# Kernel optimization log

Hardware: AMD Instinct MI355X
Metric: run time of the kernel (lower is better)

## Reference

```python
import jax, jax.numpy as jnp
import numpy as np

HID = 512
NUM_NODES = 100000
N_BATCH = 20000


def _gru_cell(x, h, W_ih, W_hh, b_ih, b_hh):
    # torch nn.GRU single-step cell; gate order r, z, n
    gi = x @ W_ih.T + b_ih            # [N, 3H]
    gh = h @ W_hh.T + b_hh            # [N, 3H]
    i_r, i_z, i_n = jnp.split(gi, 3, axis=-1)
    h_r, h_z, h_n = jnp.split(gh, 3, axis=-1)
    r = jax.nn.sigmoid(i_r + h_r)
    z = jax.nn.sigmoid(i_z + h_z)
    n = jnp.tanh(i_n + r * h_n)
    return (1.0 - z) * n + z * h


def setup_inputs() -> dict:
    key = jax.random.key(0)
    ks = jax.random.split(key, 12)
    s = 1.0 / np.sqrt(HID)
    inp = {
        'conv_emb': jax.random.normal(ks[0], (N_BATCH, HID), jnp.float32),
        'static_table': jax.random.normal(ks[1], (NUM_NODES, HID), jnp.float32),
        'dynamic_table': jax.random.normal(ks[2], (NUM_NODES, 2, HID), jnp.float32),
        'W_ih0': jax.random.normal(ks[3], (3 * HID, 2 * HID), jnp.float32) * s,
        'W_hh0': jax.random.normal(ks[4], (3 * HID, HID), jnp.float32) * s,
        'b_ih0': jax.random.normal(ks[5], (3 * HID,), jnp.float32) * s,
        'b_hh0': jax.random.normal(ks[6], (3 * HID,), jnp.float32) * s,
        'W_ih1': jax.random.normal(ks[7], (3 * HID, HID), jnp.float32) * s,
        'W_hh1': jax.random.normal(ks[8], (3 * HID, HID), jnp.float32) * s,
        'b_ih1': jax.random.normal(ks[9], (3 * HID,), jnp.float32) * s,
        'b_hh1': jax.random.normal(ks[10], (3 * HID,), jnp.float32) * s,
        'nids': jnp.arange(N_BATCH, dtype=jnp.int32),  # unique global node ids
    }
    return inp


def reference(conv_emb, static_table, dynamic_table,
              W_ih0, W_hh0, b_ih0, b_hh0,
              W_ih1, W_hh1, b_ih1, b_hh1, nids):
    # gather: static embeddings for batch nodes, concat with conv output
    x = jnp.concatenate([conv_emb, static_table[nids]], axis=-1)  # [N, 2H]
    h0 = dynamic_table[nids]                                      # [N, L, H]
    # single-step 2-layer GRU (seq_len == 1)
    h_new0 = _gru_cell(x, h0[:, 0], W_ih0, W_hh0, b_ih0, b_hh0)   # [N, H]
    h_new1 = _gru_cell(h_new0, h0[:, 1], W_ih1, W_hh1, b_ih1, b_hh1)
    hn = jnp.stack([h_new0, h_new1], axis=1)                      # [N, L, H]
    # scatter updated hidden states back into the persistent table
    updated_table = dynamic_table.at[nids].set(hn)                # [num_nodes, L, H]
    return updated_table
```

## Files before the change

### kernel.cpp

```cpp
#include <hip/hip_runtime.h>

#define NB 20000
#define NNODES 100000
#define MB2 79
#define MP2 (MB2*256)
#define NBITW 3125
#define NGEMM (MB2*8)
#define NCOPY 1416

typedef unsigned short u16;
typedef __bf16 bf16x8 __attribute__((ext_vector_type(8)));
typedef float f32x4 __attribute__((ext_vector_type(4)));

__device__ __forceinline__ u16 f2bf(float f) {
  union { float f; unsigned u; } v; v.f = f;
  unsigned r = v.u + 0x7fffu + ((v.u >> 16) & 1u);
  return (u16)(r >> 16);
}
__device__ __forceinline__ float bf2f(u16 b) {
  union { unsigned u; float f; } v; v.u = ((unsigned)b) << 16;
  return v.f;
}

template <int N> __device__ __forceinline__ void vmwaitc() {
  if constexpr (N == 0) asm volatile("s_waitcnt vmcnt(0)" ::: "memory");
  else if constexpr (N == 2) asm volatile("s_waitcnt vmcnt(2)" ::: "memory");
  else if constexpr (N == 4) asm volatile("s_waitcnt vmcnt(4)" ::: "memory");
  else asm volatile("s_waitcnt vmcnt(8)" ::: "memory");
  __builtin_amdgcn_sched_barrier(0);
}
__device__ __forceinline__ void bar() {
  __builtin_amdgcn_sched_barrier(0);
  __builtin_amdgcn_s_barrier();
  __builtin_amdgcn_sched_barrier(0);
}

__global__ void prep_bt0i(const float* __restrict__ Wih, const float* __restrict__ Whh,
                          u16* __restrict__ Bt) {
  int idx = blockIdx.x * 256 + threadIdx.x;
  if (idx >= 2048 * 384) return;
  int jg = idx / 384;
  int k = (idx % 384) * 4;
  int j = jg >> 2, g = jg & 3;
  float4 v = make_float4(0.f, 0.f, 0.f, 0.f);
  if (g < 2) {
    int row = g * 512 + j;
    v = (k < 1024) ? *(const float4*)(Wih + (size_t)row * 1024 + k)
                   : *(const float4*)(Whh + (size_t)row * 512 + (k - 1024));
  } else if (g == 2) {
    if (k < 1024) v = *(const float4*)(Wih + (size_t)(1024 + j) * 1024 + k);
  } else {
    if (k >= 1024) v = *(const float4*)(Whh + (size_t)(1024 + j) * 512 + (k - 1024));
  }
  ushort4 b; b.x = f2bf(v.x); b.y = f2bf(v.y); b.z = f2bf(v.z); b.w = f2bf(v.w);
  *(ushort4*)(Bt + (size_t)jg * 1536 + k) = b;
}

__global__ void prep_bt1i(const float* __restrict__ Wih, const float* __restrict__ Whh,
                          u16* __restrict__ Bt) {
  int idx = blockIdx.x * 256 + threadIdx.x;
  if (idx >= 2048 * 256) return;
  int jg = idx / 256;
  int k = (idx % 256) * 4;
  int j = jg >> 2, g = jg & 3;
  float4 v = make_float4(0.f, 0.f, 0.f, 0.f);
  if (g < 2) {
    int row = g * 512 + j;
    v = (k < 512) ? *(const float4*)(Wih + (size_t)row * 512 + k)
                  : *(const float4*)(Whh + (size_t)row * 512 + (k - 512));
  } else if (g == 2) {
    if (k < 512) v = *(const float4*)(Wih + (size_t)(1024 + j) * 512 + k);
  } else {
    if (k >= 512) v = *(const float4*)(Whh + (size_t)(1024 + j) * 512 + (k - 512));
  }
  ushort4 b; b.x = f2bf(v.x); b.y = f2bf(v.y); b.z = f2bf(v.z); b.w = f2bf(v.w);
  *(ushort4*)(Bt + (size_t)jg * 1024 + k) = b;
}

__global__ void prep_a(const float* __restrict__ conv, const float* __restrict__ stat,
                       const float* __restrict__ dyn, const int* __restrict__ nids,
                       u16* __restrict__ A0, u16* __restrict__ A1) {
  int idx = blockIdx.x * 256 + threadIdx.x;
  int n = idx >> 9;
  int c = (idx & 511) * 4;
  if (n >= MP2) return;
  float4 v = make_float4(0.f, 0.f, 0.f, 0.f);
  if (n < NB) {
    size_t nid = (size_t)nids[n];
    if (c < 512)        v = *(const float4*)(conv + (size_t)n * 512 + c);
    else if (c < 1024)  v = *(const float4*)(stat + nid * 512 + (c - 512));
    else if (c < 1536)  v = *(const float4*)(dyn + nid * 1024 + (c - 1024));
    else                v = *(const float4*)(dyn + nid * 1024 + 512 + (c - 1536));
  }
  ushort4 b; b.x = f2bf(v.x); b.y = f2bf(v.y); b.z = f2bf(v.z); b.w = f2bf(v.w);
  if (c < 1536) *(ushort4*)(A0 + (size_t)n * 1536 + c) = b;
  else          *(ushort4*)(A1 + (size_t)n * 1024 + (c - 1024)) = b;
  if (n >= NB && c < 512) *(ushort4*)(A1 + (size_t)n * 1024 + c) = b;
}

__global__ void zero_bits(unsigned* __restrict__ bits) {
  int i = blockIdx.x * 256 + threadIdx.x;
  if (i < NBITW) bits[i] = 0;
}
__global__ void set_bits(const int* __restrict__ nids, unsigned* __restrict__ bits) {
  int i = blockIdx.x * 256 + threadIdx.x;
  if (i < NB) {
    int nid = nids[i];
    atomicOr(&bits[nid >> 5], 1u << (nid & 31));
  }
}

template <int K, int LAYER>
__global__ __launch_bounds__(512, 2)
void gemm8(const u16* __restrict__ A, const u16* __restrict__ Bt,
           const float* __restrict__ bih, const float* __restrict__ bhh,
           const u16* __restrict__ hsrc, int hstride, const int* __restrict__ nids,
           u16* __restrict__ a1out, float* __restrict__ out,
           const float4* __restrict__ src4, float4* __restrict__ dst4,
           const unsigned* __restrict__ bits, long cbeg, long cend) {
  constexpr int NT = K / 64;
  __shared__ u16 S[4][16384];

  if (blockIdx.x >= NGEMM) {
    long cb = blockIdx.x - NGEMM;
    long total = cend - cbeg;
    long per = (total + NCOPY - 1) / NCOPY;
    long s = cbeg + cb * per;
    long e = s + per; if (e > cend) e = cend;
    long i = s + threadIdx.x;
    for (; i + 1536 < e; i += 2048) {
      float4 a0 = src4[i], a1 = src4[i + 512], a2 = src4[i + 1024], a3 = src4[i + 1536];
      int r0 = (int)(i >> 8), r1 = (int)((i + 512) >> 8),
          r2 = (int)((i + 1024) >> 8), r3 = (int)((i + 1536) >> 8);
      if (!((bits[r0 >> 5] >> (r0 & 31)) & 1u)) dst4[i] = a0;
      if (!((bits[r1 >> 5] >> (r1 & 31)) & 1u)) dst4[i + 512] = a1;
      if (!((bits[r2 >> 5] >> (r2 & 31)) & 1u)) dst4[i + 1024] = a2;
      if (!((bits[r3 >> 5] >> (r3 & 31)) & 1u)) dst4[i + 1536] = a3;
    }
    for (; i < e; i += 512) {
      int row = (int)(i >> 8);
      if (!((bits[row >> 5] >> (row & 31)) & 1u)) dst4[i] = src4[i];
    }
    return;
  }

  int bid = blockIdx.x;
  int gidx = (bid & 7) * MB2 + (bid >> 3);
  int bm = gidx >> 3, bn = gidx & 7;

  int t = threadIdx.x;
  int lane = t & 63, w = t >> 6;
  int fr = lane & 15, fq = lane >> 4;
  int wm4 = w & 3, wn = w >> 2;

  const u16* Ap = A + (size_t)bm * 256 * K;
  const u16* Bp = Bt + (size_t)bn * 256 * K;

  f32x4 acc[2][2][2][4] = {};

  auto stage = [&](int kt2, int mat, int half, const u16* gsrc) {
#pragma unroll
    for (int l = 0; l < 2; ++l) {
      int row = half * 128 + l * 64 + (t >> 3);
      int gx = ((t & 7) * 16) ^ ((row & 7) << 4);
      const u16* g = gsrc + (size_t)row * K + kt2 * 64 + (gx >> 1);
      char* lp = (char*)&S[(kt2 & 1) * 2 + mat][0] + half * 16384 + l * 8192 + t * 16;
      __builtin_amdgcn_global_load_lds((const __attribute__((address_space(1))) void*)g,
                                       (__attribute__((address_space(3))) void*)lp, 16, 0, 0);
    }
  };
  auto ld = [&](int buf, int mat, int row, int kb) -> bf16x8 {
    return *(const bf16x8*)((const char*)&S[buf * 2 + mat][0] + row * 128 +
                            (kb ^ ((row & 7) << 4)));
  };

  stage(0, 0, 0, Ap); stage(0, 1, 0, Bp); stage(0, 1, 1, Bp); stage(0, 0, 1, Ap);
  stage(1, 0, 0, Ap); stage(1, 1, 0, Bp);
  vmwaitc<8>();
  bar();

  for (int kt = 0; kt < NT; ++kt) {
    int cur = kt & 1;
#pragma unroll
    for (int q = 0; q < 4; ++q) {
      const int mh = q >> 1, nh = q & 1;
      bf16x8 af[2][2], bv[4][2];
#pragma unroll
      for (int mi = 0; mi < 2; ++mi)
#pragma unroll
        for (int ks = 0; ks < 2; ++ks)
          af[mi][ks] = ld(cur, 0, mh * 128 + wm4 * 32 + mi * 16 + fr, ks * 64 + fq * 16);
#pragma unroll
      for (int nf = 0; nf < 4; ++nf)
#pragma unroll
        for (int ks = 0; ks < 2; ++ks)
          bv[nf][ks] = ld(cur, 1, nh * 128 + wn * 64 + nf * 16 + fr, ks * 64 + fq * 16);

      if (q == 0)      { if (kt + 1 < NT) stage(kt + 1, 1, 1, Bp); }
      else if (q == 1) { if (kt + 1 < NT) stage(kt + 1, 0, 1, Ap); }
      else if (q == 2) { if (kt + 2 < NT) stage(kt + 2, 0, 0, Ap); }
      else             { if (kt + 2 < NT) stage(kt + 2, 1, 0, Bp); }

      bar();
      __builtin_amdgcn_s_setprio(1);
#pragma unroll
      for (int mi = 0; mi < 2; ++mi)
#pragma unroll
        for (int nf = 0; nf < 4; ++nf)
#pragma unroll
          for (int ks = 0; ks < 2; ++ks)
            acc[mh][nh][mi][nf] = __builtin_amdgcn_mfma_f32_16x16x32_bf16(
                af[mi][ks], bv[nf][ks], acc[mh][nh][mi][nf], 0, 0, 0);
      __builtin_amdgcn_s_setprio(0);

      if (q == 0)      { if (kt + 1 < NT) vmwaitc<8>(); else vmwaitc<2>(); }
      else if (q == 1) { if (kt + 1 < NT) vmwaitc<8>(); else vmwaitc<0>(); }
      else if (q == 3) { if (kt + 1 < NT) { if (kt + 2 < NT) vmwaitc<8>(); else vmwaitc<4>(); } }
      bar();
    }
  }

  int gg = fr & 3, jj = fr >> 2;
  float bias[2][4];
#pragma unroll
  for (int nh = 0; nh < 2; ++nh)
#pragma unroll
    for (int nf = 0; nf < 4; ++nf) {
      int j = ((bn * 256 + nh * 128 + wn * 64 + nf * 16) >> 2) + jj;
      bias[nh][nf] = (gg == 0) ? bih[j] + bhh[j]
                   : (gg == 1) ? bih[512 + j] + bhh[512 + j]
                   : (gg == 2) ? bih[1024 + j] : bhh[1024 + j];
    }
#pragma unroll
  for (int mh = 0; mh < 2; ++mh)
#pragma unroll
    for (int nh = 0; nh < 2; ++nh)
#pragma unroll
      for (int mi = 0; mi < 2; ++mi) {
        int row = bm * 256 + mh * 128 + wm4 * 32 + mi * 16 + fq * 4 + gg;
#pragma unroll
        for (int nf = 0; nf < 4; ++nf) {
          float v[4], v1[4], v2[4];
#pragma unroll
          for (int r = 0; r < 4; ++r) v[r] = acc[mh][nh][mi][nf][r] + bias[nh][nf];
#pragma unroll
          for (int i = 0; i < 4; ++i) {
            float o = __shfl_xor(v[i ^ 2], 2);
            v1[i] = ((i ^ gg) & 2) ? o : v[i];
          }
#pragma unroll
          for (int i = 0; i < 4; ++i) {
            float o = __shfl_xor(v1[i ^ 1], 1);
            v2[i] = ((i ^ gg) & 1) ? o : v1[i];
          }
          if (row < NB) {
            int j = ((bn * 256 + nh * 128 + wn * 64 + nf * 16) >> 2) + jj;
            float rr = 1.f / (1.f + __expf(-v2[0]));
            float zz = 1.f / (1.f + __expf(-v2[1]));
            float nn = tanhf(fmaf(rr, v2[3], v2[2]));
            float h = bf2f(hsrc[(size_t)row * hstride + j]);
            float hp = (1.f - zz) * nn + zz * h;
            if (LAYER == 0) a1out[(size_t)row * 1024 + j] = f2bf(hp);
            out[(size_t)nids[row] * 1024 + LAYER * 512 + j] = hp;
          }
        }
      }
}

__global__ void copy_tail(const float4* __restrict__ src, float4* __restrict__ dst,
                          const unsigned* __restrict__ bits, long cbeg, long cend) {
  for (long i = cbeg + (long)blockIdx.x * 256 + threadIdx.x; i < cend;
       i += (long)gridDim.x * 256) {
    int row = (int)(i >> 8);
    if (!((bits[row >> 5] >> (row & 31)) & 1u)) dst[i] = src[i];
  }
}

extern "C" void kernel_launch(void* const* d_in, const int* in_sizes, int n_in,
                              void* d_out, int out_size, void* d_ws, size_t ws_size,
                              hipStream_t stream) {
  const float* conv = (const float*)d_in[0];
  const float* stat = (const float*)d_in[1];
  const float* dyn  = (const float*)d_in[2];
  const float* Wih0 = (const float*)d_in[3];
  const float* Whh0 = (const float*)d_in[4];
  const float* bih0 = (const float*)d_in[5];
  const float* bhh0 = (const float*)d_in[6];
  const float* Wih1 = (const float*)d_in[7];
  const float* Whh1 = (const float*)d_in[8];
  const float* bih1 = (const float*)d_in[9];
  const float* bhh1 = (const float*)d_in[10];
  const int*   nids = (const int*)d_in[11];
  float* out = (float*)d_out;

  char* ws = (char*)d_ws;
  u16* A0  = (u16*)ws;
  u16* A1  = (u16*)(ws + 62128128);
  u16* Bt0 = (u16*)(ws + 103546880);
  u16* Bt1 = (u16*)(ws + 109838336);
  unsigned* bits = (unsigned*)(ws + 114032640);

  zero_bits<<<(NBITW + 255) / 256, 256, 0, stream>>>(bits);
  set_bits<<<(NB + 255) / 256, 256, 0, stream>>>(nids, bits);
  prep_bt0i<<<3072, 256, 0, stream>>>(Wih0, Whh0, Bt0);
  prep_bt1i<<<2048, 256, 0, stream>>>(Wih1, Whh1, Bt1);
  prep_a<<<(MP2 * 512) / 256, 256, 0, stream>>>(conv, stat, dyn, nids, A0, A1);

  const long E_ROW = 256;
  gemm8<1536, 0><<<NGEMM + NCOPY, 512, 0, stream>>>(
      A0, Bt0, bih0, bhh0, A0 + 1024, 1536, nids, A1, out,
      (const float4*)dyn, (float4*)out, bits, 0L, 55000L * E_ROW);
  gemm8<1024, 1><<<NGEMM + NCOPY, 512, 0, stream>>>(
      A1, Bt1, bih1, bhh1, A1 + 512, 1024, nids, (u16*)nullptr, out,
      (const float4*)dyn, (float4*)out, bits, 55000L * E_ROW, 92000L * E_ROW);
  copy_tail<<<1024, 256, 0, stream>>>((const float4*)dyn, (float4*)out, bits,
                                      92000L * E_ROW, (long)NNODES * E_ROW);
}
```

Before: 510.2 us.

## Rewrite GEMM as K=32 four-stage pipeline and move table copy to separate kernel

Replaces the 256x256 GEMM main loop with a K-step of 32, a four-deep LDS ring buffer and a new swizzled staging layout with an 8x4 MFMA tile per wave. The copy blocks that were fused into the GEMM grids are removed, along with the grouped block-index remapping. The copy of untouched dynamic-table rows now runs as one standalone kernel after both GEMMs. This simplifies the GEMM schedule and deepens prefetch, but the copy bandwidth no longer overlaps with GEMM compute.

```diff
diff --git a/kernel.cpp b/kernel.cpp
--- a/kernel.cpp
+++ b/kernel.cpp
@@ -6,7 +6,6 @@
 #define MP2 (MB2*256)
 #define NBITW 3125
 #define NGEMM (MB2*8)
-#define NCOPY 1416
 
 typedef unsigned short u16;
 typedef __bf16 bf16x8 __attribute__((ext_vector_type(8)));
@@ -24,7 +23,6 @@
 
 template <int N> __device__ __forceinline__ void vmwaitc() {
   if constexpr (N == 0) asm volatile("s_waitcnt vmcnt(0)" ::: "memory");
-  else if constexpr (N == 2) asm volatile("s_waitcnt vmcnt(2)" ::: "memory");
   else if constexpr (N == 4) asm volatile("s_waitcnt vmcnt(4)" ::: "memory");
   else asm volatile("s_waitcnt vmcnt(8)" ::: "memory");
   __builtin_amdgcn_sched_barrier(0);
@@ -112,165 +110,136 @@
 
 template <int K, int LAYER>
 __global__ __launch_bounds__(512, 2)
-void gemm8(const u16* __restrict__ A, const u16* __restrict__ Bt,
+void gemm4(const u16* __restrict__ A, const u16* __restrict__ Bt,
            const float* __restrict__ bih, const float* __restrict__ bhh,
            const u16* __restrict__ hsrc, int hstride, const int* __restrict__ nids,
-           u16* __restrict__ a1out, float* __restrict__ out,
-           const float4* __restrict__ src4, float4* __restrict__ dst4,
-           const unsigned* __restrict__ bits, long cbeg, long cend) {
-  constexpr int NT = K / 64;
+           u16* __restrict__ a1out, float* __restrict__ out) {
+  constexpr int NT = K / 32;
   __shared__ u16 S[4][16384];
 
-  if (blockIdx.x >= NGEMM) {
-    long cb = blockIdx.x - NGEMM;
-    long total = cend - cbeg;
-    long per = (total + NCOPY - 1) / NCOPY;
-    long s = cbeg + cb * per;
-    long e = s + per; if (e > cend) e = cend;
-    long i = s + threadIdx.x;
-    for (; i + 1536 < e; i += 2048) {
-      float4 a0 = src4[i], a1 = src4[i + 512], a2 = src4[i + 1024], a3 = src4[i + 1536];
-      int r0 = (int)(i >> 8), r1 = (int)((i + 512) >> 8),
-          r2 = (int)((i + 1024) >> 8), r3 = (int)((i + 1536) >> 8);
-      if (!((bits[r0 >> 5] >> (r0 & 31)) & 1u)) dst4[i] = a0;
-      if (!((bits[r1 >> 5] >> (r1 & 31)) & 1u)) dst4[i + 512] = a1;
-      if (!((bits[r2 >> 5] >> (r2 & 31)) & 1u)) dst4[i + 1024] = a2;
-      if (!((bits[r3 >> 5] >> (r3 & 31)) & 1u)) dst4[i + 1536] = a3;
-    }
-    for (; i < e; i += 512) {
-      int row = (int)(i >> 8);
-      if (!((bits[row >> 5] >> (row & 31)) & 1u)) dst4[i] = src4[i];
-    }
-    return;
-  }
-
   int bid = blockIdx.x;
-  int gidx = (bid & 7) * MB2 + (bid >> 3);
-  int bm = gidx >> 3, bn = gidx & 7;
+  int bn = bid & 7, bm = bid >> 3;
 
   int t = threadIdx.x;
   int lane = t & 63, w = t >> 6;
   int fr = lane & 15, fq = lane >> 4;
-  int wm4 = w & 3, wn = w >> 2;
+  int wm = w >> 2, wn = w & 3;
 
   const u16* Ap = A + (size_t)bm * 256 * K;
   const u16* Bp = Bt + (size_t)bn * 256 * K;
 
-  f32x4 acc[2][2][2][4] = {};
-
-  auto stage = [&](int kt2, int mat, int half, const u16* gsrc) {
-#pragma unroll
-    for (int l = 0; l < 2; ++l) {
-      int row = half * 128 + l * 64 + (t >> 3);
-      int gx = ((t & 7) * 16) ^ ((row & 7) << 4);
-      const u16* g = gsrc + (size_t)row * K + kt2 * 64 + (gx >> 1);
-      char* lp = (char*)&S[(kt2 & 1) * 2 + mat][0] + half * 16384 + l * 8192 + t * 16;
+  int goff[4]; int gsel[4];
+  {
+#pragma unroll
+    for (int l = 0; l < 4; ++l) {
+      int c = l * 512 + t;
+      gsel[l] = c >> 10;
+      int cm = c & 1023;
+      int pair = cm >> 3, s = cm & 7;
+      int u = s ^ (pair & 7);
+      int row = pair * 2 + (u & 1);
+      goff[l] = row * K + (u >> 1) * 8;
+    }
+  }
+  auto stage = [&](int kt) {
+    char* base = (char*)S + (size_t)(kt & 3) * 32768;
+#pragma unroll
+    for (int l = 0; l < 4; ++l) {
+      const u16* g = (gsel[l] ? Bp : Ap) + goff[l] + kt * 32;
       __builtin_amdgcn_global_load_lds((const __attribute__((address_space(1))) void*)g,
-                                       (__attribute__((address_space(3))) void*)lp, 16, 0, 0);
+                                       (__attribute__((address_space(3))) void*)
+                                       (base + (l * 512 + t) * 16), 16, 0, 0);
     }
   };
-  auto ld = [&](int buf, int mat, int row, int kb) -> bf16x8 {
-    return *(const bf16x8*)((const char*)&S[buf * 2 + mat][0] + row * 128 +
-                            (kb ^ ((row & 7) << 4)));
-  };
-
-  stage(0, 0, 0, Ap); stage(0, 1, 0, Bp); stage(0, 1, 1, Bp); stage(0, 0, 1, Ap);
-  stage(1, 0, 0, Ap); stage(1, 1, 0, Bp);
+
+  int offA[8], offB[4];
+#pragma unroll
+  for (int mi = 0; mi < 8; ++mi)
+    offA[mi] = (wm * 64 + mi * 8 + (fr >> 1)) * 128 +
+               (((fq * 2 + (fr & 1)) ^ (fr >> 1)) << 4);
+#pragma unroll
+  for (int nf = 0; nf < 4; ++nf)
+    offB[nf] = 16384 + (wn * 32 + nf * 8 + (fr >> 1)) * 128 +
+               (((fq * 2 + (fr & 1)) ^ (fr >> 1)) << 4);
+
+  f32x4 acc[8][4] = {};
+
+  stage(0); stage(1); stage(2);
   vmwaitc<8>();
   bar();
 
   for (int kt = 0; kt < NT; ++kt) {
-    int cur = kt & 1;
-#pragma unroll
-    for (int q = 0; q < 4; ++q) {
-      const int mh = q >> 1, nh = q & 1;
-      bf16x8 af[2][2], bv[4][2];
-#pragma unroll
-      for (int mi = 0; mi < 2; ++mi)
-#pragma unroll
-        for (int ks = 0; ks < 2; ++ks)
-          af[mi][ks] = ld(cur, 0, mh * 128 + wm4 * 32 + mi * 16 + fr, ks * 64 + fq * 16);
+    const char* sb = (const char*)S + (size_t)(kt & 3) * 32768;
+    bf16x8 bv[4], af[8];
+#pragma unroll
+    for (int nf = 0; nf < 4; ++nf) bv[nf] = *(const bf16x8*)(sb + offB[nf]);
+#pragma unroll
+    for (int mi = 0; mi < 8; ++mi) af[mi] = *(const bf16x8*)(sb + offA[mi]);
+
+    if (kt + 3 < NT) stage(kt + 3);
+
+    bar();
+    __builtin_amdgcn_s_setprio(1);
+#pragma unroll
+    for (int mi = 0; mi < 8; ++mi)
 #pragma unroll
       for (int nf = 0; nf < 4; ++nf)
-#pragma unroll
-        for (int ks = 0; ks < 2; ++ks)
-          bv[nf][ks] = ld(cur, 1, nh * 128 + wn * 64 + nf * 16 + fr, ks * 64 + fq * 16);
-
-      if (q == 0)      { if (kt + 1 < NT) stage(kt + 1, 1, 1, Bp); }
-      else if (q == 1) { if (kt + 1 < NT) stage(kt + 1, 0, 1, Ap); }
-      else if (q == 2) { if (kt + 2 < NT) stage(kt + 2, 0, 0, Ap); }
-      else             { if (kt + 2 < NT) stage(kt + 2, 1, 0, Bp); }
-
-      bar();
-      __builtin_amdgcn_s_setprio(1);
-#pragma unroll
-      for (int mi = 0; mi < 2; ++mi)
-#pragma unroll
-        for (int nf = 0; nf < 4; ++nf)
-#pragma unroll
-          for (int ks = 0; ks < 2; ++ks)
-            acc[mh][nh][mi][nf] = __builtin_amdgcn_mfma_f32_16x16x32_bf16(
-                af[mi][ks], bv[nf][ks], acc[mh][nh][mi][nf], 0, 0, 0);
-      __builtin_amdgcn_s_setprio(0);
-
-      if (q == 0)      { if (kt + 1 < NT) vmwaitc<8>(); else vmwaitc<2>(); }
-      else if (q == 1) { if (kt + 1 < NT) vmwaitc<8>(); else vmwaitc<0>(); }
-      else if (q == 3) { if (kt + 1 < NT) { if (kt + 2 < NT) vmwaitc<8>(); else vmwaitc<4>(); } }
-      bar();
+        acc[mi][nf] = __builtin_amdgcn_mfma_f32_16x16x32_bf16(af[mi], bv[nf],
+                                                              acc[mi][nf], 0, 0, 0);
+    __builtin_amdgcn_s_setprio(0);
+
+    if (kt < NT - 3)       vmwaitc<8>();
+    else if (kt == NT - 3) vmwaitc<4>();
+    else if (kt == NT - 2) vmwaitc<0>();
+    bar();
+  }
+
+  int gg = fr & 3, jj = fr >> 2;
+  float bias[4];
+#pragma unroll
+  for (int nf = 0; nf < 4; ++nf) {
+    int j = bn * 64 + wn * 16 + nf * 4 + jj;
+    bias[nf] = (gg == 0) ? bih[j] + bhh[j]
+             : (gg == 1) ? bih[512 + j] + bhh[512 + j]
+             : (gg == 2) ? bih[1024 + j] : bhh[1024 + j];
+  }
+#pragma unroll
+  for (int mi = 0; mi < 8; ++mi) {
+    int row = bm * 256 + wm * 128 + mi * 16 + fq * 4 + gg;
+#pragma unroll
+    for (int nf = 0; nf < 4; ++nf) {
+      float v[4], v1[4], v2[4];
+#pragma unroll
+      for (int r = 0; r < 4; ++r) v[r] = acc[mi][nf][r] + bias[nf];
+#pragma unroll
+      for (int i = 0; i < 4; ++i) {
+        float o = __shfl_xor(v[i ^ 2], 2);
+        v1[i] = ((i ^ gg) & 2) ? o : v[i];
+      }
+#pragma unroll
+      for (int i = 0; i < 4; ++i) {
+        float o = __shfl_xor(v1[i ^ 1], 1);
+        v2[i] = ((i ^ gg) & 1) ? o : v1[i];
+      }
+      if (row < NB) {
+        int j = bn * 64 + wn * 16 + nf * 4 + jj;
+        float rr = 1.f / (1.f + __expf(-v2[0]));
+        float zz = 1.f / (1.f + __expf(-v2[1]));
+        float nn = tanhf(fmaf(rr, v2[3], v2[2]));
+        float h = bf2f(hsrc[(size_t)row * hstride + j]);
+        float hp = (1.f - zz) * nn + zz * h;
+        if (LAYER == 0) a1out[(size_t)row * 1024 + j] = f2bf(hp);
+        out[(size_t)nids[row] * 1024 + LAYER * 512 + j] = hp;
+      }
     }
   }
-
-  int gg = fr & 3, jj = fr >> 2;
-  float bias[2][4];
-#pragma unroll
-  for (int nh = 0; nh < 2; ++nh)
-#pragma unroll
-    for (int nf = 0; nf < 4; ++nf) {
-      int j = ((bn * 256 + nh * 128 + wn * 64 + nf * 16) >> 2) + jj;
-      bias[nh][nf] = (gg == 0) ? bih[j] + bhh[j]
-                   : (gg == 1) ? bih[512 + j] + bhh[512 + j]
-                   : (gg == 2) ? bih[1024 + j] : bhh[1024 + j];
-    }
-#pragma unroll
-  for (int mh = 0; mh < 2; ++mh)
-#pragma unroll
-    for (int nh = 0; nh < 2; ++nh)
-#pragma unroll
-      for (int mi = 0; mi < 2; ++mi) {
-        int row = bm * 256 + mh * 128 + wm4 * 32 + mi * 16 + fq * 4 + gg;
-#pragma unroll
-        for (int nf = 0; nf < 4; ++nf) {
-          float v[4], v1[4], v2[4];
-#pragma unroll
-          for (int r = 0; r < 4; ++r) v[r] = acc[mh][nh][mi][nf][r] + bias[nh][nf];
-#pragma unroll
-          for (int i = 0; i < 4; ++i) {
-            float o = __shfl_xor(v[i ^ 2], 2);
-            v1[i] = ((i ^ gg) & 2) ? o : v[i];
-          }
-#pragma unroll
-          for (int i = 0; i < 4; ++i) {
-            float o = __shfl_xor(v1[i ^ 1], 1);
-            v2[i] = ((i ^ gg) & 1) ? o : v1[i];
-          }
-          if (row < NB) {
-            int j = ((bn * 256 + nh * 128 + wn * 64 + nf * 16) >> 2) + jj;
-            float rr = 1.f / (1.f + __expf(-v2[0]));
-            float zz = 1.f / (1.f + __expf(-v2[1]));
-            float nn = tanhf(fmaf(rr, v2[3], v2[2]));
-            float h = bf2f(hsrc[(size_t)row * hstride + j]);
-            float hp = (1.f - zz) * nn + zz * h;
-            if (LAYER == 0) a1out[(size_t)row * 1024 + j] = f2bf(hp);
-            out[(size_t)nids[row] * 1024 + LAYER * 512 + j] = hp;
-          }
-        }
-      }
-}
-
-__global__ void copy_tail(const float4* __restrict__ src, float4* __restrict__ dst,
-                          const unsigned* __restrict__ bits, long cbeg, long cend) {
-  for (long i = cbeg + (long)blockIdx.x * 256 + threadIdx.x; i < cend;
-       i += (long)gridDim.x * 256) {
+}
+
+__global__ void copy_skip(const float4* __restrict__ src, float4* __restrict__ dst,
+                          const unsigned* __restrict__ bits) {
+  const size_t total = (size_t)NNODES * 256;
+  for (size_t i = (size_t)blockIdx.x * 256 + threadIdx.x; i < total;
+       i += (size_t)gridDim.x * 256) {
     int row = (int)(i >> 8);
     if (!((bits[row >> 5] >> (row & 31)) & 1u)) dst[i] = src[i];
   }
@@ -306,13 +275,10 @@
   prep_bt1i<<<2048, 256, 0, stream>>>(Wih1, Whh1, Bt1);
   prep_a<<<(MP2 * 512) / 256, 256, 0, stream>>>(conv, stat, dyn, nids, A0, A1);
 
-  const long E_ROW = 256;
-  gemm8<1536, 0><<<NGEMM + NCOPY, 512, 0, stream>>>(
-      A0, Bt0, bih0, bhh0, A0 + 1024, 1536, nids, A1, out,
-      (const float4*)dyn, (float4*)out, bits, 0L, 55000L * E_ROW);
-  gemm8<1024, 1><<<NGEMM + NCOPY, 512, 0, stream>>>(
-      A1, Bt1, bih1, bhh1, A1 + 512, 1024, nids, (u16*)nullptr, out,
-      (const float4*)dyn, (float4*)out, bits, 55000L * E_ROW, 92000L * E_ROW);
-  copy_tail<<<1024, 256, 0, stream>>>((const float4*)dyn, (float4*)out, bits,
-                                      92000L * E_ROW, (long)NNODES * E_ROW);
-}
+  gemm4<1536, 0><<<NGEMM, 512, 0, stream>>>(A0, Bt0, bih0, bhh0,
+                                            A0 + 1024, 1536, nids, A1, out);
+  gemm4<1024, 1><<<NGEMM, 512, 0, stream>>>(A1, Bt1, bih1, bhh1,
+                                            A1 + 512, 1024, nids, (u16*)nullptr, out);
+
+  copy_skip<<<2048, 256, 0, stream>>>((const float4*)dyn, (float4*)out, bits);
+}
```

Result: slower. 537.7 us (+5.4%).
